# Optimization experiments

Measured on AMD Instinct MI355X. Metric: run time of the kernel, lower is better.

Reference implementation:

```python
import jax, jax.numpy as jnp
import numpy as np

B, T, NS, NC, M = 256, 128, 12, 4, 6
MU = 0.1                 # barrier parameter alg.mu
REG_BASE = 1.6           # fp.reg_exp_base
REG = 2.0                # bp.reg
REG_FAC = REG_BASE ** REG - 1.0


def _mt(a):
    return jnp.swapaxes(a, -1, -2)


def setup_inputs():
    key = jax.random.key(0)
    k = jax.random.split(key, 18)
    rn = lambda i, shape: jax.random.normal(k[i], shape, dtype=jnp.float32)
    eye_s = jnp.eye(NS, dtype=jnp.float32)
    eye_c = jnp.eye(NC, dtype=jnp.float32)
    fx = 0.9 * eye_s + 0.02 * rn(0, (B, T, NS, NS))
    fu = 0.1 * rn(1, (B, T, NS, NC))
    fxx = 0.01 * rn(2, (B, T, NS, NS, NS))
    fxu = 0.01 * rn(3, (B, T, NS, NS, NC))
    fuu = 0.01 * rn(4, (B, T, NS, NC, NC))
    qx = 0.1 * rn(5, (B, T, NS))
    qu = 0.1 * rn(6, (B, T, NC))
    Ax = 0.1 * rn(7, (B, T, NS, NS))
    qxx = eye_s + Ax @ _mt(Ax)            # PSD stage cost Hessian
    Au = 0.1 * rn(8, (B, T, NC, NC))
    quu = eye_c + Au @ _mt(Au)            # PD control Hessian
    qxu = 0.05 * rn(9, (B, T, NS, NC))
    cx = 0.1 * rn(10, (B, T, M, NS))
    cu = 0.1 * rn(11, (B, T, M, NC))
    # feasible iterate: c < 0 strictly, dual s > 0
    c = -(jax.random.uniform(k[12], (B, T, M), dtype=jnp.float32) + 0.1)
    s = 0.05 + 0.1 * jax.random.uniform(k[13], (B, T, M), dtype=jnp.float32)
    px = 0.1 * rn(14, (B, NS))
    P = 0.1 * rn(15, (B, NS, NS))
    pxx = eye_s + P @ _mt(P)              # PSD terminal Hessian
    return {"qx": qx, "qu": qu, "qxx": qxx, "qxu": qxu, "quu": quu,
            "fx": fx, "fu": fu, "fxx": fxx, "fxu": fxu, "fuu": fuu,
            "cx": cx, "cu": cu, "c": c, "s": s, "px": px, "pxx": pxx}


def _backward_pass(qx, qu, qxx, qxu, quu, fx, fu, fxx, fxu, fuu, cx, cu, c, s, px, pxx):
    """Feasible-branch ipddp Riccati backward recursion over T steps, batched over B."""
    Bsz = qx.shape[0]

    def step(carry, inp):
        Vx, Vxx, dV0, dV1, qu_err, mu_err = carry
        (qx_t, qu_t, qxx_t, qxu_t, quu_t, fx_t, fu_t,
         fxx_t, fxu_t, fuu_t, cx_t, cu_t, c_t, s_t) = inp
        s_col = s_t[..., None]                      # (B,M,1)
        c_col = c_t[..., None]                      # (B,M,1)
        # Q-function expansions
        Qx = qx_t[..., None] + _mt(cx_t) @ s_col + _mt(fx_t) @ Vx       # (B,NS,1)
        Qu = qu_t[..., None] + _mt(cu_t) @ s_col + _mt(fu_t) @ Vx       # (B,NC,1)
        fxV = _mt(fx_t) @ Vxx
        v = Vx[..., 0]                              # (B,NS)
        Qxx = qxx_t + fxV @ fx_t + jnp.einsum('bs,bsij->bij', v, fxx_t)
        Qxu = qxu_t + fxV @ fu_t + jnp.einsum('bs,bsij->bij', v, fxu_t)
        Quu = quu_t + _mt(fu_t) @ Vxx @ fu_t + jnp.einsum('bs,bsij->bij', v, fuu_t)
        Quu = 0.5 * (Quu + _mt(Quu))
        Quu_reg = Quu + quu_t * REG_FAC
        # interior-point (feasible) modifications
        r = s_col * c_col + MU                      # (B,M,1)
        cinv = 1.0 / c_col
        sc = (s_t / c_t)[..., None]                 # diag(SCinv) entries
        SCcu = sc * cu_t                            # SCinv @ cu
        SCcx = sc * cx_t                            # SCinv @ cx
        cuSCcu = _mt(cu_t) @ SCcu
        Qu = Qu - _mt(cu_t) @ (cinv * r)
        tempQux = _mt(Qxu) - _mt(cu_t) @ SCcx       # (B,NC,NS)
        rhs = jnp.concatenate([Qu, tempQux], axis=-1)   # (B,NC,1+NS)
        kK = -jnp.linalg.solve(Quu_reg - cuSCcu, rhs)
        ku = kK[..., :1]                            # (B,NC,1)
        Ku = kK[..., 1:]                            # (B,NC,NS)
        cuku = cu_t @ ku                            # (B,M,1)
        ks = (-cinv * (r + s_col * cuku))[..., 0]   # (B,M)
        Ks = -(sc * (cx_t + cu_t @ Ku))             # (B,M,NS)
        Quu2 = Quu - cuSCcu
        Qxu2 = _mt(tempQux)
        Qxx2 = Qxx - _mt(cx_t) @ SCcx
        Qx2 = Qx - _mt(cx_t) @ (cinv * r)
        dV0 = dV0 + (_mt(ku) @ Qu)[..., 0, 0]
        dV1 = dV1 + 0.5 * (_mt(ku) @ Quu2 @ ku)[..., 0, 0]
        QxuKu = Qxu2 @ Ku
        KtQ = _mt(Ku) @ Quu2
        Vx_new = Qx2 + _mt(Ku) @ Qu + KtQ @ ku + Qxu2 @ ku
        Vxx_new = Qxx2 + _mt(QxuKu) + QxuKu + KtQ @ Ku
        Vxx_new = 0.5 * (Vxx_new + _mt(Vxx_new))
        qu_err = jnp.maximum(qu_err, jnp.max(jnp.abs(Qu)))
        mu_err = jnp.maximum(mu_err, jnp.max(jnp.abs(r)))
        return (Vx_new, Vxx_new, dV0, dV1, qu_err, mu_err), (ku[..., 0], Ku, ks, Ks)

    xs = tuple(jnp.moveaxis(a, 1, 0) for a in
               (qx, qu, qxx, qxu, quu, fx, fu, fxx, fxu, fuu, cx, cu, c, s))
    zero = jnp.zeros((), jnp.float32)
    init = (px[..., None], pxx, jnp.zeros((Bsz,), jnp.float32),
            jnp.zeros((Bsz,), jnp.float32), zero, zero)
    carry, outs = jax.lax.scan(step, init, xs, reverse=True)
    Vx, Vxx, dV0, dV1, qu_err, mu_err = carry
    ku, Ku, ks, Ks = (jnp.moveaxis(o, 0, 1) for o in outs)
    dV = jnp.stack([dV0, dV1], axis=-1)             # (B,2)
    opterr = jnp.maximum(qu_err, mu_err)            # c_err == 0 in feasible branch
    return ku, Ku, ks, Ks, dV, opterr, Vx[..., 0], Vxx


def reference(qx, qu, qxx, qxu, quu, fx, fu, fxx, fxu, fuu, cx, cu, c, s, px, pxx):
    return _backward_pass(qx, qu, qxx, qxu, quu, fx, fu, fxx, fxu, fuu,
                          cx, cu, c, s, px, pxx)
```

## Files before the change

### kernel.cpp

```cpp
#include <hip/hip_runtime.h>
#include <cstdint>
#include <cstddef>

#define B_  256
#define T_  128
#define NS_ 12
#define NC_ 4
#define M_  6

constexpr float MU_F      = 0.1f;
constexpr float REG_FAC_F = (float)(1.6 * 1.6 - 1.0);

#define OF_FX   0
#define OF_FU   144
#define OF_FXX  192
#define OF_FXU  1920
#define OF_FUU  2496
#define OF_QXX  2688
#define OF_QXU  2832
#define OF_QUU  2880
#define OF_QX   2896
#define OF_QU   2908
#define OF_CX   2912
#define OF_CU   2984
#define OF_C    3008
#define OF_S    3014
#define STG_N   3020

#define O_KU    0
#define O_KUBIG 131072
#define O_KS    1703936
#define O_KSBIG 1900544
#define O_DV    4259840
#define O_OPT   4260352
#define O_VX    4260353
#define O_VXX   4263425

__device__ __forceinline__ void wsync_lds() {
    asm volatile("s_waitcnt lgkmcnt(0)" ::: "memory");
}
__device__ __forceinline__ void wsync_all() {
    asm volatile("s_waitcnt vmcnt(0) lgkmcnt(0)" ::: "memory");
}

__device__ __forceinline__ void gl_lds16(const float* g, float* l) {
    __builtin_amdgcn_global_load_lds((const __attribute__((address_space(1))) void*)g,
                                     (__attribute__((address_space(3))) void*)l, 16, 0, 0);
}
__device__ __forceinline__ void gl_lds4(const float* g, float* l) {
    __builtin_amdgcn_global_load_lds((const __attribute__((address_space(1))) void*)g,
                                     (__attribute__((address_space(3))) void*)l, 4, 0, 0);
}
__device__ __forceinline__ float4 ld4(const float* p)  { return *reinterpret_cast<const float4*>(p); }
__device__ __forceinline__ void   st4(float* p, float4 v) { *reinterpret_cast<float4*>(p) = v; }

__global__ __launch_bounds__(64) void ddp_backward(
    const float* __restrict__ qx,  const float* __restrict__ qu,
    const float* __restrict__ qxx, const float* __restrict__ qxu,
    const float* __restrict__ quu, const float* __restrict__ fx,
    const float* __restrict__ fu,  const float* __restrict__ fxx,
    const float* __restrict__ fxu, const float* __restrict__ fuu,
    const float* __restrict__ cx,  const float* __restrict__ cu,
    const float* __restrict__ c_,  const float* __restrict__ s_,
    const float* __restrict__ px,  const float* __restrict__ pxx,
    float* __restrict__ out, float* __restrict__ ws)
{
    const int l = threadIdx.x;
    const int b = blockIdx.x;

    __shared__ alignas(16) float stg[2][STG_N];
    __shared__ alignas(16) float sVxe[192];
    __shared__ alignas(16) float sG[192];
    __shared__ alignas(16) float sOUT[192];
    __shared__ alignas(16) float sQuuR[16], sQuu2[16], sM4[16];
    __shared__ alignas(16) float sQP[16];
    __shared__ alignas(16) float sKu[48];
    __shared__ alignas(16) float sku[4];
    __shared__ alignas(16) float sR[8], sCINV[8], sSC[8];
    __shared__ float sAcc[4];

    const float* srcs[14] = {qx, qu, qxx, qxu, quu, fx, fu, fxx, fxu, fuu, cx, cu, c_, s_};

    const int p   = l & 15, cq = l >> 4;
    const bool cq3 = (cq == 3);
    const int u1_x  = (p < 12) ? (OF_FX + p) : (OF_FU + p - 12);
    const int u1_xs = (p < 12) ? 12 : 4;
    const int u1_q0 = (p < 12) ? (OF_QX + p) : (OF_QU + p - 12);
    const int u1_w  = (p < 12) ? (OF_CX + p) : (OF_CU + p - 12);
    const int u1_ws = (p < 12) ? 12 : 4;
    const int pr = l >> 2, q4 = l & 3;
    const bool q43 = (q4 == 3);
    const int u2_q0 = (pr < 12) ? (q43 ? (OF_QXU + pr * 4) : (OF_QXX + pr * 12 + q4 * 4))
                                : (OF_QUU + (pr - 12) * 4);
    const int u2_x  = q43 ? OF_FU : (OF_FX + q4 * 4);
    const int u2_xs = q43 ? 4 : 12;
    const int u2_t  = (pr < 12) ? (q43 ? (OF_FXU + pr * 4) : (OF_FXX + pr * 12 + q4 * 4))
                                : (OF_FUU + (pr - 12) * 4);
    const int u2_ts = (pr < 12) ? (q43 ? 48 : 144) : 16;
    const int u2_w  = q43 ? OF_CU : (OF_CX + q4 * 4);
    const int u2_ws = q43 ? 4 : 12;
    const int i5 = l / 3, jq5 = l % 3;

    auto prefetch = [&](float* dst, int tt) {
        const uint32_t bt2 = (uint32_t)b * T_ + (uint32_t)tt;
        constexpr int ch_arr[22]  = {5,6,7,7,7,7,7,7,7,8,8,8,9,2,3,4,0,1,10,11,12,13};
        constexpr int ch_goff[22] = {0,0,0,256,512,768,1024,1280,1536,0,256,512,0,0,0,0,0,0,0,0,0,0};
        constexpr int ch_loff[22] = {OF_FX, OF_FU,
                                     OF_FXX, OF_FXX+256, OF_FXX+512, OF_FXX+768,
                                     OF_FXX+1024, OF_FXX+1280, OF_FXX+1536,
                                     OF_FXU, OF_FXU+256, OF_FXU+512,
                                     OF_FUU, OF_QXX, OF_QXU, OF_QUU, OF_QX, OF_QU,
                                     OF_CX, OF_CU, OF_C, OF_S};
        constexpr int ch_nb[22]   = {576,192,1024,1024,1024,1024,1024,1024,768,
                                     1024,1024,256,768,576,192,64,48,16,288,96,24,24};
        constexpr int sl[14]      = {12,4,144,48,16,144,48,1728,576,192,72,24,6,6};
        #pragma unroll
        for (int ci = 0; ci < 22; ++ci) {
            const uint32_t off = bt2 * (uint32_t)sl[ch_arr[ci]] + (uint32_t)ch_goff[ci];
            const float* g = srcs[ch_arr[ci]] + (size_t)off;
            float* dl = dst + ch_loff[ci];
            if ((ch_nb[ci] & 15) == 0) {
                if (l * 16 < ch_nb[ci]) gl_lds16(g + l * 4, dl);
            } else {
                if (l * 4  < ch_nb[ci]) gl_lds4 (g + l,     dl);
            }
        }
    };

    #pragma unroll
    for (int idx = l; idx < 192; idx += 64) {
        const int r = idx >> 4, ci = idx & 15;
        float v = 0.f;
        if (ci < 12)       v = pxx[(size_t)b * 144 + r * 12 + ci];
        else if (ci == 12) v = px[(size_t)b * 12 + r];
        sVxe[idx] = v;
    }
    prefetch(stg[0], T_ - 1);
    wsync_all();

    float dv0 = 0.f, dv1 = 0.f, qerr = 0.f, merr = 0.f;
    int cur = 0;
    for (int t = T_ - 1; t >= 0; --t) {
        const float* S = stg[cur];
        const uint32_t bt = (uint32_t)b * T_ + (uint32_t)t;

        float fcol[12];
        float4 vrow[12];
        #pragma unroll
        for (int m = 0; m < 12; ++m) fcol[m] = S[u1_x + m * u1_xs];
        #pragma unroll
        for (int m = 0; m < 12; ++m) vrow[m] = ld4(sVxe + m * 16 + cq * 4);
        const float4 csq0 = ld4(S + OF_C);
        const float4 csq1 = ld4(S + OF_C + 4);
        const float4 csq2 = ld4(S + OF_C + 8);
        float4 u2f[12];
        #pragma unroll
        for (int k = 0; k < 12; ++k) u2f[k] = ld4(S + u2_x + k * u2_xs);
        const float4 u2q0 = ld4(S + u2_q0);
        float4 u2tv[12];
        #pragma unroll
        for (int s2 = 0; s2 < 12; ++s2) u2tv[s2] = ld4(S + u2_t + s2 * u2_ts);

        if (t > 0) prefetch(stg[cur ^ 1], t - 1);

        {
            if (cq3 && p < 6) {
                const float cc = S[OF_C + p], sv = S[OF_S + p];
                sR[p]    = sv * cc + MU_F;
                sCINV[p] = 1.0f / cc;
                sSC[p]   = sv / cc;
            }
            float accx = 0.f, accy = 0.f, accz = 0.f, accw = 0.f;
            if (cq3) {
                float a0 = S[u1_q0];
                #pragma unroll
                for (int k = 0; k < 6; ++k) a0 += S[u1_w + k * u1_ws] * S[OF_S + k];
                accx = a0;
            }
            #pragma unroll
            for (int m = 0; m < 12; ++m) {
                const float f = fcol[m];
                accx += f * vrow[m].x; accy += f * vrow[m].y;
                accz += f * vrow[m].z; accw += f * vrow[m].w;
            }
            if (!cq3) {
                st4(sG + p * 12 + cq * 4, make_float4(accx, accy, accz, accw));
            } else {
                const float cv[6] = {csq0.x, csq0.y, csq0.z, csq0.w, csq1.x, csq1.y};
                const float sv[6] = {csq1.z, csq1.w, csq2.x, csq2.y, csq2.z, csq2.w};
                float rck[6], rrk[6];
                #pragma unroll
                for (int k = 0; k < 6; ++k) { rck[k] = 1.0f / cv[k]; rrk[k] = sv[k] * cv[k] + MU_F; }
                #pragma unroll
                for (int k = 0; k < 6; ++k) accx -= S[u1_w + k * u1_ws] * rck[k] * rrk[k];
                sQP[p] = accx;
            }
        }
        wsync_lds();

        {
            float vx[12];
            #pragma unroll
            for (int m = 0; m < 12; ++m) vx[m] = sVxe[m * 16 + 12];
            float rsc[6];
            #pragma unroll
            for (int k = 0; k < 6; ++k) rsc[k] = sSC[k];

            const float4 g0 = ld4(sG + pr * 12);
            const float4 g1 = ld4(sG + pr * 12 + 4);
            const float4 g2 = ld4(sG + pr * 12 + 8);
            const float gk[12] = {g0.x,g0.y,g0.z,g0.w, g1.x,g1.y,g1.z,g1.w, g2.x,g2.y,g2.z,g2.w};

            float4 acc = u2q0;
            #pragma unroll
            for (int k = 0; k < 12; ++k) {
                const float4 f = u2f[k];
                acc.x += gk[k]*f.x; acc.y += gk[k]*f.y; acc.z += gk[k]*f.z; acc.w += gk[k]*f.w;
            }
            #pragma unroll
            for (int s2 = 0; s2 < 12; ++s2) {
                const float4 tv = u2tv[s2];
                acc.x += vx[s2]*tv.x; acc.y += vx[s2]*tv.y; acc.z += vx[s2]*tv.z; acc.w += vx[s2]*tv.w;
            }
            if (pr < 12) {
                #pragma unroll
                for (int k = 0; k < 6; ++k) {
                    const float t2 = rsc[k] * S[OF_CX + k * 12 + pr];
                    const float4 cv = ld4(S + u2_w + k * u2_ws);
                    acc.x -= t2*cv.x; acc.y -= t2*cv.y; acc.z -= t2*cv.z; acc.w -= t2*cv.w;
                }
                st4(sOUT + pr * 16 + q4 * 4, acc);
            } else if (q43) {
                st4(sQuuR + (pr - 12) * 4, acc);
            }
            wsync_lds();
            if (pr >= 12 && q43) {
                const int a = pr - 12;
                const float accq[4] = {acc.x, acc.y, acc.z, acc.w};
                float q2v[4];
                #pragma unroll
                for (int bb = 0; bb < 4; ++bb) {
                    const float q = 0.5f * (accq[bb] + sQuuR[bb * 4 + a]);
                    float cs2 = 0.f;
                    #pragma unroll
                    for (int k = 0; k < 6; ++k)
                        cs2 += rsc[k] * S[OF_CU + k*4 + a] * S[OF_CU + k*4 + bb];
                    q2v[bb] = q - cs2;
                }
                const float4 quuq = ld4(S + OF_QUU + a * 4);
                st4(sQuu2 + a * 4, make_float4(q2v[0], q2v[1], q2v[2], q2v[3]));
                st4(sM4   + a * 4, make_float4(q2v[0] + quuq.x * REG_FAC_F,
                                               q2v[1] + quuq.y * REG_FAC_F,
                                               q2v[2] + quuq.z * REG_FAC_F,
                                               q2v[3] + quuq.w * REG_FAC_F));
            }
        }
        wsync_lds();

        if (l < 13) {
            float a00=sM4[0],  a01=sM4[1],  a02=sM4[2],  a03=sM4[3];
            float a10=sM4[4],  a11=sM4[5],  a12=sM4[6],  a13=sM4[7];
            float a20=sM4[8],  a21=sM4[9],  a22=sM4[10], a23=sM4[11];
            float a30=sM4[12], a31=sM4[13], a32=sM4[14], a33=sM4[15];
            const float i0 = 1.0f / a00;
            const float l10 = a10*i0, l20 = a20*i0, l30 = a30*i0;
            a11 -= l10*a01; a12 -= l10*a02; a13 -= l10*a03;
            a21 -= l20*a01; a22 -= l20*a02; a23 -= l20*a03;
            a31 -= l30*a01; a32 -= l30*a02; a33 -= l30*a03;
            const float i1 = 1.0f / a11;
            const float l21 = a21*i1, l31 = a31*i1;
            a22 -= l21*a12; a23 -= l21*a13;
            a32 -= l31*a12; a33 -= l31*a13;
            const float i2 = 1.0f / a22;
            const float l32 = a32*i2;
            a33 -= l32*a23;

            float r0, r1, r2, r3;
            if (l == 0) { const float4 q = ld4(sQP + 12);             r0=q.x; r1=q.y; r2=q.z; r3=q.w; }
            else        { const float4 q = ld4(sOUT + (l-1)*16 + 12); r0=q.x; r1=q.y; r2=q.z; r3=q.w; }

            const float y0 = r0;
            const float y1 = r1 - l10*y0;
            const float y2 = r2 - l20*y0 - l21*y1;
            const float y3 = r3 - l30*y0 - l31*y1 - l32*y2;
            float x3 = y3 / a33;
            float x2 = (y2 - a23*x3) * i2;
            float x1 = (y1 - a12*x2 - a13*x3) * i1;
            float x0 = (y0 - a01*x1 - a02*x2 - a03*x3) * i0;
            x0 = -x0; x1 = -x1; x2 = -x2; x3 = -x3;

            if (l == 0) {
                sku[0]=x0; sku[1]=x1; sku[2]=x2; sku[3]=x3;
                st4(out + O_KU + (size_t)bt * 4, make_float4(x0, x1, x2, x3));
                const float kux[4] = {x0, x1, x2, x3};
                float d0 = 0.f;
                #pragma unroll
                for (int a = 0; a < 4; ++a) d0 += kux[a] * sQP[12 + a];
                dv0 += d0;
                float d1 = 0.f;
                #pragma unroll
                for (int a = 0; a < 4; ++a)
                    #pragma unroll
                    for (int b2 = 0; b2 < 4; ++b2) d1 += kux[a] * sQuu2[a*4 + b2] * kux[b2];
                dv1 += 0.5f * d1;
            } else {
                const int i = l - 1;
                sKu[i]=x0; sKu[12+i]=x1; sKu[24+i]=x2; sKu[36+i]=x3;
                float* Kg = out + O_KUBIG + (size_t)bt * 48;
                Kg[i]=x0; Kg[12+i]=x1; Kg[24+i]=x2; Kg[36+i]=x3;
            }
        } else if (l == 20) {
            float m = 0.f;
            #pragma unroll
            for (int a = 0; a < 4; ++a) m = fmaxf(m, fabsf(sQP[12 + a]));
            qerr = fmaxf(qerr, m);
        } else if (l == 21) {
            float m = 0.f;
            #pragma unroll
            for (int k = 0; k < 6; ++k) m = fmaxf(m, fabsf(sR[k]));
            merr = fmaxf(merr, m);
        }
        wsync_lds();

        if (l < 18) {
            const int k = i5, iq = jq5;
            const float4 cxv = ld4(S + OF_CX + k*12 + iq*4);
            float a0 = cxv.x, a1 = cxv.y, a2 = cxv.z, a3v = cxv.w;
            #pragma unroll
            for (int a = 0; a < 4; ++a) {
                const float  cua = S[OF_CU + k*4 + a];
                const float4 kv  = ld4(sKu + a*12 + iq*4);
                a0 += cua*kv.x; a1 += cua*kv.y; a2 += cua*kv.z; a3v += cua*kv.w;
            }
            const float ns = -sSC[k];
            st4(out + O_KSBIG + (size_t)bt * 72 + k*12 + iq*4,
                make_float4(ns*a0, ns*a1, ns*a2, ns*a3v));
            if (iq == 0) {
                float cuku = 0.f;
                #pragma unroll
                for (int a = 0; a < 4; ++a) cuku += S[OF_CU + k*4 + a] * sku[a];
                out[O_KS + (size_t)bt * 6 + k] = -sCINV[k] * (sR[k] + S[OF_S + k] * cuku);
            }
        }
        if (l < 36) {
            const int i = i5, jq = jq5;
            const float4 v14  = ld4(sOUT + i*16 + jq*4);
            const float4 tqi4 = ld4(sOUT + i*16 + 12);
            const float tqi[4] = {tqi4.x, tqi4.y, tqi4.z, tqi4.w};
            float kuj[4][4], kui[4];
            #pragma unroll
            for (int a = 0; a < 4; ++a) {
                const float4 kv = ld4(sKu + a*12 + jq*4);
                kuj[a][0]=kv.x; kuj[a][1]=kv.y; kuj[a][2]=kv.z; kuj[a][3]=kv.w;
                kui[a] = sKu[a*12 + i];
            }
            float4 q2r[4];
            #pragma unroll
            for (int bb = 0; bb < 4; ++bb) q2r[bb] = ld4(sQuu2 + bb*4);
            float kqi[4] = {0.f, 0.f, 0.f, 0.f};
            #pragma unroll
            for (int bb = 0; bb < 4; ++bb) {
                kqi[0] += kui[bb]*q2r[bb].x; kqi[1] += kui[bb]*q2r[bb].y;
                kqi[2] += kui[bb]*q2r[bb].z; kqi[3] += kui[bb]*q2r[bb].w;
            }
            float kqj[4][4];
            #pragma unroll
            for (int r = 0; r < 4; ++r) { kqj[r][0]=0.f; kqj[r][1]=0.f; kqj[r][2]=0.f; kqj[r][3]=0.f; }
            #pragma unroll
            for (int bb = 0; bb < 4; ++bb) {
                #pragma unroll
                for (int r = 0; r < 4; ++r) {
                    kqj[r][0] += kuj[bb][r]*q2r[bb].x; kqj[r][1] += kuj[bb][r]*q2r[bb].y;
                    kqj[r][2] += kuj[bb][r]*q2r[bb].z; kqj[r][3] += kuj[bb][r]*q2r[bb].w;
                }
            }
            const float v1a[4] = {v14.x, v14.y, v14.z, v14.w};
            float v2[4], tqj[4][4];
            #pragma unroll
            for (int r = 0; r < 4; ++r) {
                const int j = jq*4 + r;
                v2[r] = sOUT[j*16 + i];
                const float4 tq = ld4(sOUT + j*16 + 12);
                tqj[r][0]=tq.x; tqj[r][1]=tq.y; tqj[r][2]=tq.z; tqj[r][3]=tq.w;
            }
            float res[4];
            #pragma unroll
            for (int r = 0; r < 4; ++r) {
                float qk = 0.f, kk1 = 0.f, kk2 = 0.f;
                #pragma unroll
                for (int a = 0; a < 4; ++a) {
                    qk  += tqi[a]*kuj[a][r] + tqj[r][a]*kui[a];
                    kk1 += kqi[a]*kuj[a][r];
                    kk2 += kqj[r][a]*kui[a];
                }
                res[r] = 0.5f*(v1a[r] + v2[r]) + qk + 0.5f*(kk1 + kk2);
            }
            st4(sVxe + i*16 + jq*4, make_float4(res[0], res[1], res[2], res[3]));
        } else if (l < 48) {
            const int i = l - 36;
            float kub[4];
            #pragma unroll
            for (int bb = 0; bb < 4; ++bb) kub[bb] = sKu[bb*12 + i];
            float4 q2r[4];
            #pragma unroll
            for (int bb = 0; bb < 4; ++bb) q2r[bb] = ld4(sQuu2 + bb*4);
            float ktq[4] = {0.f, 0.f, 0.f, 0.f};
            #pragma unroll
            for (int bb = 0; bb < 4; ++bb) {
                ktq[0] += kub[bb]*q2r[bb].x; ktq[1] += kub[bb]*q2r[bb].y;
                ktq[2] += kub[bb]*q2r[bb].z; ktq[3] += kub[bb]*q2r[bb].w;
            }
            float acc = sQP[i];
            #pragma unroll
            for (int a = 0; a < 4; ++a)
                acc += kub[a]*sQP[12+a] + ktq[a]*sku[a] + sOUT[i*16+12+a]*sku[a];
            st4(sVxe + i*16 + 12, make_float4(acc, 0.f, 0.f, 0.f));
        }
        wsync_all();
        cur ^= 1;
    }

    if (l == 20) sAcc[2] = qerr;
    if (l == 21) sAcc[3] = merr;
    wsync_lds();
    if (l == 0) {
        out[O_DV + b*2 + 0] = dv0;
        out[O_DV + b*2 + 1] = dv1;
        ws[b] = fmaxf(sAcc[2], sAcc[3]);
    }
    if (l < 12) out[O_VX + b*12 + l] = sVxe[l*16 + 12];
    #pragma unroll
    for (int idx = l; idx < 144; idx += 64)
        out[O_VXX + (size_t)b*144 + idx] = sVxe[(idx/12)*16 + (idx%12)];
}

__global__ __launch_bounds__(256) void opt_reduce(const float* __restrict__ ws,
                                                  float* __restrict__ out)
{
    float v = ws[threadIdx.x];
    #pragma unroll
    for (int o = 32; o > 0; o >>= 1) v = fmaxf(v, __shfl_down(v, o, 64));
    __shared__ float m[4];
    if ((threadIdx.x & 63) == 0) m[threadIdx.x >> 6] = v;
    __syncthreads();
    if (threadIdx.x == 0) out[O_OPT] = fmaxf(fmaxf(m[0], m[1]), fmaxf(m[2], m[3]));
}

extern "C" void kernel_launch(void* const* d_in, const int* in_sizes, int n_in,
                              void* d_out, int out_size, void* d_ws, size_t ws_size,
                              hipStream_t stream) {
    const float* qx  = (const float*)d_in[0];
    const float* qu  = (const float*)d_in[1];
    const float* qxx = (const float*)d_in[2];
    const float* qxu = (const float*)d_in[3];
    const float* quu = (const float*)d_in[4];
    const float* fx  = (const float*)d_in[5];
    const float* fu  = (const float*)d_in[6];
    const float* fxx = (const float*)d_in[7];
    const float* fxu = (const float*)d_in[8];
    const float* fuu = (const float*)d_in[9];
    const float* cx  = (const float*)d_in[10];
    const float* cu  = (const float*)d_in[11];
    const float* c_  = (const float*)d_in[12];
    const float* s_  = (const float*)d_in[13];
    const float* px  = (const float*)d_in[14];
    const float* pxx = (const float*)d_in[15];
    float* out = (float*)d_out;
    float* ws  = (float*)d_ws;

    hipLaunchKernelGGL(ddp_backward, dim3(B_), dim3(64), 0, stream,
                       qx, qu, qxx, qxu, quu, fx, fu, fxx, fxu, fuu,
                       cx, cu, c_, s_, px, pxx, out, ws);
    hipLaunchKernelGGL(opt_reduce, dim3(1), dim3(256), 0, stream, ws, out);
}
```

Before: 729.7 us.

## Split backward step into compute wave and prefetch/output wave per block

Launches two wavefronts per block. Wave 0 runs the serial Riccati critical path (Q expansion, 4x4 LU solve, Vxx update), while wave 1 issues the next timestep's global-to-LDS prefetch and writes the ks/Ks outputs, dV and error terms. Work is handed between waves with s_barrier. The aim is to take global memory issue and output stores off the latency-bound critical wave, at the cost of two block barriers per step and extra threads.

Result: faster. 691.2 us (-5.3%).

```diff
diff --git a/kernel.cpp b/kernel.cpp
--- a/kernel.cpp
+++ b/kernel.cpp
@@ -54,7 +54,7 @@
 __device__ __forceinline__ float4 ld4(const float* p)  { return *reinterpret_cast<const float4*>(p); }
 __device__ __forceinline__ void   st4(float* p, float4 v) { *reinterpret_cast<float4*>(p) = v; }
 
-__global__ __launch_bounds__(64) void ddp_backward(
+__global__ __launch_bounds__(128) void ddp_backward(
     const float* __restrict__ qx,  const float* __restrict__ qu,
     const float* __restrict__ qxx, const float* __restrict__ qxu,
     const float* __restrict__ quu, const float* __restrict__ fx,
@@ -65,14 +65,16 @@
     const float* __restrict__ px,  const float* __restrict__ pxx,
     float* __restrict__ out, float* __restrict__ ws)
 {
-    const int l = threadIdx.x;
-    const int b = blockIdx.x;
+    const int tid = threadIdx.x;
+    const int l   = tid & 63;
+    const int wv  = tid >> 6;
+    const int b   = blockIdx.x;
 
     __shared__ alignas(16) float stg[2][STG_N];
     __shared__ alignas(16) float sVxe[192];
     __shared__ alignas(16) float sG[192];
     __shared__ alignas(16) float sOUT[192];
-    __shared__ alignas(16) float sQuuR[16], sQuu2[16], sM4[16];
+    __shared__ alignas(16) float sQuu2[16], sM4[16];
     __shared__ alignas(16) float sQP[16];
     __shared__ alignas(16) float sKu[48];
     __shared__ alignas(16) float sku[4];
@@ -127,16 +129,21 @@
         }
     };
 
-    #pragma unroll
-    for (int idx = l; idx < 192; idx += 64) {
-        const int r = idx >> 4, ci = idx & 15;
-        float v = 0.f;
-        if (ci < 12)       v = pxx[(size_t)b * 144 + r * 12 + ci];
-        else if (ci == 12) v = px[(size_t)b * 12 + r];
-        sVxe[idx] = v;
+    if (wv == 0) {
+        #pragma unroll
+        for (int idx = l; idx < 192; idx += 64) {
+            const int r = idx >> 4, ci = idx & 15;
+            float v = 0.f;
+            if (ci < 12)       v = pxx[(size_t)b * 144 + r * 12 + ci];
+            else if (ci == 12) v = px[(size_t)b * 12 + r];
+            sVxe[idx] = v;
+        }
+        wsync_lds();
+    } else {
+        prefetch(stg[0], T_ - 1);
+        wsync_all();
     }
-    prefetch(stg[0], T_ - 1);
-    wsync_all();
+    __builtin_amdgcn_s_barrier();
 
     float dv0 = 0.f, dv1 = 0.f, qerr = 0.f, merr = 0.f;
     int cur = 0;
@@ -144,294 +151,314 @@
         const float* S = stg[cur];
         const uint32_t bt = (uint32_t)b * T_ + (uint32_t)t;
 
-        float fcol[12];
-        float4 vrow[12];
-        #pragma unroll
-        for (int m = 0; m < 12; ++m) fcol[m] = S[u1_x + m * u1_xs];
-        #pragma unroll
-        for (int m = 0; m < 12; ++m) vrow[m] = ld4(sVxe + m * 16 + cq * 4);
-        const float4 csq0 = ld4(S + OF_C);
-        const float4 csq1 = ld4(S + OF_C + 4);
-        const float4 csq2 = ld4(S + OF_C + 8);
-        float4 u2f[12];
-        #pragma unroll
-        for (int k = 0; k < 12; ++k) u2f[k] = ld4(S + u2_x + k * u2_xs);
-        const float4 u2q0 = ld4(S + u2_q0);
-        float4 u2tv[12];
-        #pragma unroll
-        for (int s2 = 0; s2 < 12; ++s2) u2tv[s2] = ld4(S + u2_t + s2 * u2_ts);
-
-        if (t > 0) prefetch(stg[cur ^ 1], t - 1);
-
-        {
-            if (cq3 && p < 6) {
-                const float cc = S[OF_C + p], sv = S[OF_S + p];
-                sR[p]    = sv * cc + MU_F;
-                sCINV[p] = 1.0f / cc;
-                sSC[p]   = sv / cc;
-            }
-            float accx = 0.f, accy = 0.f, accz = 0.f, accw = 0.f;
-            if (cq3) {
-                float a0 = S[u1_q0];
-                #pragma unroll
-                for (int k = 0; k < 6; ++k) a0 += S[u1_w + k * u1_ws] * S[OF_S + k];
-                accx = a0;
-            }
+        if (wv == 1) {
+            if (t > 0) prefetch(stg[cur ^ 1], t - 1);
+        } else {
+            float fcol[12];
+            float4 vrow[12];
             #pragma unroll
-            for (int m = 0; m < 12; ++m) {
-                const float f = fcol[m];
-                accx += f * vrow[m].x; accy += f * vrow[m].y;
-                accz += f * vrow[m].z; accw += f * vrow[m].w;
-            }
-            if (!cq3) {
-                st4(sG + p * 12 + cq * 4, make_float4(accx, accy, accz, accw));
-            } else {
-                const float cv[6] = {csq0.x, csq0.y, csq0.z, csq0.w, csq1.x, csq1.y};
-                const float sv[6] = {csq1.z, csq1.w, csq2.x, csq2.y, csq2.z, csq2.w};
-                float rck[6], rrk[6];
-                #pragma unroll
-                for (int k = 0; k < 6; ++k) { rck[k] = 1.0f / cv[k]; rrk[k] = sv[k] * cv[k] + MU_F; }
-                #pragma unroll
-                for (int k = 0; k < 6; ++k) accx -= S[u1_w + k * u1_ws] * rck[k] * rrk[k];
-                sQP[p] = accx;
-            }
+            for (int m = 0; m < 12; ++m) fcol[m] = S[u1_x + m * u1_xs];
+            #pragma unroll
+            for (int m = 0; m < 12; ++m) vrow[m] = ld4(sVxe + m * 16 + cq * 4);
+            const float4 csq0 = ld4(S + OF_C);
+            const float4 csq1 = ld4(S + OF_C + 4);
+            const float4 csq2 = ld4(S + OF_C + 8);
+            float4 u2f[12];
+            #pragma unroll
+            for (int k = 0; k < 12; ++k) u2f[k] = ld4(S + u2_x + k * u2_xs);
+            const float4 u2q0 = ld4(S + u2_q0);
+            float4 u2tv[12];
+            #pragma unroll
+            for (int s2 = 0; s2 < 12; ++s2) u2tv[s2] = ld4(S + u2_t + s2 * u2_ts);
+
+            {
+                if (cq3 && p < 6) {
+                    const float cc = S[OF_C + p], sv = S[OF_S + p];
+                    sR[p]    = sv * cc + MU_F;
+                    sCINV[p] = 1.0f / cc;
+                    sSC[p]   = sv / cc;
+                }
+                float accx = 0.f, accy = 0.f, accz = 0.f, accw = 0.f;
+                if (cq3) {
+                    float a0 = S[u1_q0];
+                    #pragma unroll
+                    for (int k = 0; k < 6; ++k) a0 += S[u1_w + k * u1_ws] * S[OF_S + k];
+                    accx = a0;
+                }
+                #pragma unroll
+                for (int m = 0; m < 12; ++m) {
+                    const float f = fcol[m];
+                    accx += f * vrow[m].x; accy += f * vrow[m].y;
+                    accz += f * vrow[m].z; accw += f * vrow[m].w;
+                }
+                if (!cq3) {
+                    st4(sG + p * 12 + cq * 4, make_float4(accx, accy, accz, accw));
+                } else {
+                    const float cv6[6] = {csq0.x, csq0.y, csq0.z, csq0.w, csq1.x, csq1.y};
+                    const float sv6[6] = {csq1.z, csq1.w, csq2.x, csq2.y, csq2.z, csq2.w};
+                    float rck[6], rrk[6];
+                    #pragma unroll
+                    for (int k = 0; k < 6; ++k) { rck[k] = 1.0f / cv6[k]; rrk[k] = sv6[k] * cv6[k] + MU_F; }
+                    #pragma unroll
+                    for (int k = 0; k < 6; ++k) accx -= S[u1_w + k * u1_ws] * rck[k] * rrk[k];
+                    sQP[p] = accx;
+                }
+            }
+            wsync_lds();
+
+            {
+                float vx[12];
+                #pragma unroll
+                for (int m = 0; m < 12; ++m) vx[m] = sVxe[m * 16 + 12];
+                float rsc[6];
+                #pragma unroll
+                for (int k = 0; k < 6; ++k) rsc[k] = sSC[k];
+
+                const float4 g0 = ld4(sG + pr * 12);
+                const float4 g1 = ld4(sG + pr * 12 + 4);
+                const float4 g2 = ld4(sG + pr * 12 + 8);
+                const float gk[12] = {g0.x,g0.y,g0.z,g0.w, g1.x,g1.y,g1.z,g1.w, g2.x,g2.y,g2.z,g2.w};
+
+                float4 acc = u2q0;
+                #pragma unroll
+                for (int k = 0; k < 12; ++k) {
+                    const float4 f = u2f[k];
+                    acc.x += gk[k]*f.x; acc.y += gk[k]*f.y; acc.z += gk[k]*f.z; acc.w += gk[k]*f.w;
+                }
+                #pragma unroll
+                for (int s2 = 0; s2 < 12; ++s2) {
+                    const float4 tv = u2tv[s2];
+                    acc.x += vx[s2]*tv.x; acc.y += vx[s2]*tv.y; acc.z += vx[s2]*tv.z; acc.w += vx[s2]*tv.w;
+                }
+                if (pr < 12) {
+                    #pragma unroll
+                    for (int k = 0; k < 6; ++k) {
+                        const float t2 = rsc[k] * S[OF_CX + k * 12 + pr];
+                        const float4 cv = ld4(S + u2_w + k * u2_ws);
+                        acc.x -= t2*cv.x; acc.y -= t2*cv.y; acc.z -= t2*cv.z; acc.w -= t2*cv.w;
+                    }
+                    st4(sOUT + pr * 16 + q4 * 4, acc);
+                } else if (q43) {
+                    const int a = pr - 12;
+                    const float accq[4] = {acc.x, acc.y, acc.z, acc.w};
+                    float q2v[4];
+                    #pragma unroll
+                    for (int bb = 0; bb < 4; ++bb) {
+                        float cacc = S[OF_QUU + bb*4 + a];
+                        #pragma unroll
+                        for (int k = 0; k < 12; ++k)
+                            cacc += sG[(12 + bb) * 12 + k] * S[OF_FU + k*4 + a];
+                        #pragma unroll
+                        for (int s2 = 0; s2 < 12; ++s2)
+                            cacc += vx[s2] * S[OF_FUU + s2*16 + bb*4 + a];
+                        const float q = 0.5f * (accq[bb] + cacc);
+                        float cs2 = 0.f;
+                        #pragma unroll
+                        for (int k = 0; k < 6; ++k)
+                            cs2 += rsc[k] * S[OF_CU + k*4 + a] * S[OF_CU + k*4 + bb];
+                        q2v[bb] = q - cs2;
+                    }
+                    const float4 quuq = ld4(S + OF_QUU + a * 4);
+                    st4(sQuu2 + a * 4, make_float4(q2v[0], q2v[1], q2v[2], q2v[3]));
+                    st4(sM4   + a * 4, make_float4(q2v[0] + quuq.x * REG_FAC_F,
+                                                   q2v[1] + quuq.y * REG_FAC_F,
+                                                   q2v[2] + quuq.z * REG_FAC_F,
+                                                   q2v[3] + quuq.w * REG_FAC_F));
+                }
+            }
+            wsync_lds();
+
+            if (l < 13) {
+                float a00=sM4[0],  a01=sM4[1],  a02=sM4[2],  a03=sM4[3];
+                float a10=sM4[4],  a11=sM4[5],  a12=sM4[6],  a13=sM4[7];
+                float a20=sM4[8],  a21=sM4[9],  a22=sM4[10], a23=sM4[11];
+                float a30=sM4[12], a31=sM4[13], a32=sM4[14], a33=sM4[15];
+                const float i0 = 1.0f / a00;
+                const float l10 = a10*i0, l20 = a20*i0, l30 = a30*i0;
+                a11 -= l10*a01; a12 -= l10*a02; a13 -= l10*a03;
+                a21 -= l20*a01; a22 -= l20*a02; a23 -= l20*a03;
+                a31 -= l30*a01; a32 -= l30*a02; a33 -= l30*a03;
+                const float i1 = 1.0f / a11;
+                const float l21 = a21*i1, l31 = a31*i1;
+                a22 -= l21*a12; a23 -= l21*a13;
+                a32 -= l31*a12; a33 -= l31*a13;
+                const float i2 = 1.0f / a22;
+                const float l32 = a32*i2;
+                a33 -= l32*a23;
+
+                float r0, r1, r2, r3;
+                if (l == 0) { const float4 q = ld4(sQP + 12);             r0=q.x; r1=q.y; r2=q.z; r3=q.w; }
+                else        { const float4 q = ld4(sOUT + (l-1)*16 + 12); r0=q.x; r1=q.y; r2=q.z; r3=q.w; }
+
+                const float y0 = r0;
+                const float y1 = r1 - l10*y0;
+                const float y2 = r2 - l20*y0 - l21*y1;
+                const float y3 = r3 - l30*y0 - l31*y1 - l32*y2;
+                float x3 = y3 / a33;
+                float x2 = (y2 - a23*x3) * i2;
+                float x1 = (y1 - a12*x2 - a13*x3) * i1;
+                float x0 = (y0 - a01*x1 - a02*x2 - a03*x3) * i0;
+                x0 = -x0; x1 = -x1; x2 = -x2; x3 = -x3;
+
+                if (l == 0) { sku[0]=x0; sku[1]=x1; sku[2]=x2; sku[3]=x3; }
+                else {
+                    const int i = l - 1;
+                    sKu[i]=x0; sKu[12+i]=x1; sKu[24+i]=x2; sKu[36+i]=x3;
+                }
+            }
+            wsync_lds();
         }
-        wsync_lds();
-
-        {
-            float vx[12];
-            #pragma unroll
-            for (int m = 0; m < 12; ++m) vx[m] = sVxe[m * 16 + 12];
-            float rsc[6];
-            #pragma unroll
-            for (int k = 0; k < 6; ++k) rsc[k] = sSC[k];
-
-            const float4 g0 = ld4(sG + pr * 12);
-            const float4 g1 = ld4(sG + pr * 12 + 4);
-            const float4 g2 = ld4(sG + pr * 12 + 8);
-            const float gk[12] = {g0.x,g0.y,g0.z,g0.w, g1.x,g1.y,g1.z,g1.w, g2.x,g2.y,g2.z,g2.w};
-
-            float4 acc = u2q0;
-            #pragma unroll
-            for (int k = 0; k < 12; ++k) {
-                const float4 f = u2f[k];
-                acc.x += gk[k]*f.x; acc.y += gk[k]*f.y; acc.z += gk[k]*f.z; acc.w += gk[k]*f.w;
-            }
-            #pragma unroll
-            for (int s2 = 0; s2 < 12; ++s2) {
-                const float4 tv = u2tv[s2];
-                acc.x += vx[s2]*tv.x; acc.y += vx[s2]*tv.y; acc.z += vx[s2]*tv.z; acc.w += vx[s2]*tv.w;
-            }
-            if (pr < 12) {
-                #pragma unroll
-                for (int k = 0; k < 6; ++k) {
-                    const float t2 = rsc[k] * S[OF_CX + k * 12 + pr];
-                    const float4 cv = ld4(S + u2_w + k * u2_ws);
-                    acc.x -= t2*cv.x; acc.y -= t2*cv.y; acc.z -= t2*cv.z; acc.w -= t2*cv.w;
-                }
-                st4(sOUT + pr * 16 + q4 * 4, acc);
-            } else if (q43) {
-                st4(sQuuR + (pr - 12) * 4, acc);
+        __builtin_amdgcn_s_barrier();
+
+        if (wv == 0) {
+            if (l < 36) {
+                const int i = i5, jq = jq5;
+                const float4 v14  = ld4(sOUT + i*16 + jq*4);
+                const float4 tqi4 = ld4(sOUT + i*16 + 12);
+                const float tqi[4] = {tqi4.x, tqi4.y, tqi4.z, tqi4.w};
+                float kuj[4][4], kui[4];
+                #pragma unroll
+                for (int a = 0; a < 4; ++a) {
+                    const float4 kv = ld4(sKu + a*12 + jq*4);
+                    kuj[a][0]=kv.x; kuj[a][1]=kv.y; kuj[a][2]=kv.z; kuj[a][3]=kv.w;
+                    kui[a] = sKu[a*12 + i];
+                }
+                float4 q2r[4];
+                #pragma unroll
+                for (int bb = 0; bb < 4; ++bb) q2r[bb] = ld4(sQuu2 + bb*4);
+                float kqi[4] = {0.f, 0.f, 0.f, 0.f};
+                #pragma unroll
+                for (int bb = 0; bb < 4; ++bb) {
+                    kqi[0] += kui[bb]*q2r[bb].x; kqi[1] += kui[bb]*q2r[bb].y;
+                    kqi[2] += kui[bb]*q2r[bb].z; kqi[3] += kui[bb]*q2r[bb].w;
+                }
+                float kqj[4][4];
+                #pragma unroll
+                for (int r = 0; r < 4; ++r) { kqj[r][0]=0.f; kqj[r][1]=0.f; kqj[r][2]=0.f; kqj[r][3]=0.f; }
+                #pragma unroll
+                for (int bb = 0; bb < 4; ++bb) {
+                    #pragma unroll
+                    for (int r = 0; r < 4; ++r) {
+                        kqj[r][0] += kuj[bb][r]*q2r[bb].x; kqj[r][1] += kuj[bb][r]*q2r[bb].y;
+                        kqj[r][2] += kuj[bb][r]*q2r[bb].z; kqj[r][3] += kuj[bb][r]*q2r[bb].w;
+                    }
+                }
+                const float v1a[4] = {v14.x, v14.y, v14.z, v14.w};
+                float v2[4], tqj[4][4];
+                #pragma unroll
+                for (int r = 0; r < 4; ++r) {
+                    const int j = jq*4 + r;
+                    v2[r] = sOUT[j*16 + i];
+                    const float4 tq = ld4(sOUT + j*16 + 12);
+                    tqj[r][0]=tq.x; tqj[r][1]=tq.y; tqj[r][2]=tq.z; tqj[r][3]=tq.w;
+                }
+                float res[4];
+                #pragma unroll
+                for (int r = 0; r < 4; ++r) {
+                    float qk = 0.f, kk1 = 0.f, kk2 = 0.f;
+                    #pragma unroll
+                    for (int a = 0; a < 4; ++a) {
+                        qk  += tqi[a]*kuj[a][r] + tqj[r][a]*kui[a];
+                        kk1 += kqi[a]*kuj[a][r];
+                        kk2 += kqj[r][a]*kui[a];
+                    }
+                    res[r] = 0.5f*(v1a[r] + v2[r]) + qk + 0.5f*(kk1 + kk2);
+                }
+                st4(sVxe + i*16 + jq*4, make_float4(res[0], res[1], res[2], res[3]));
+            } else if (l < 48) {
+                const int i = l - 36;
+                float kub[4];
+                #pragma unroll
+                for (int bb = 0; bb < 4; ++bb) kub[bb] = sKu[bb*12 + i];
+                float4 q2r[4];
+                #pragma unroll
+                for (int bb = 0; bb < 4; ++bb) q2r[bb] = ld4(sQuu2 + bb*4);
+                float ktq[4] = {0.f, 0.f, 0.f, 0.f};
+                #pragma unroll
+                for (int bb = 0; bb < 4; ++bb) {
+                    ktq[0] += kub[bb]*q2r[bb].x; ktq[1] += kub[bb]*q2r[bb].y;
+                    ktq[2] += kub[bb]*q2r[bb].z; ktq[3] += kub[bb]*q2r[bb].w;
+                }
+                float acc = sQP[i];
+                #pragma unroll
+                for (int a = 0; a < 4; ++a)
+                    acc += kub[a]*sQP[12+a] + ktq[a]*sku[a] + sOUT[i*16+12+a]*sku[a];
+                st4(sVxe + i*16 + 12, make_float4(acc, 0.f, 0.f, 0.f));
             }
             wsync_lds();
-            if (pr >= 12 && q43) {
-                const int a = pr - 12;
-                const float accq[4] = {acc.x, acc.y, acc.z, acc.w};
-                float q2v[4];
-                #pragma unroll
-                for (int bb = 0; bb < 4; ++bb) {
-                    const float q = 0.5f * (accq[bb] + sQuuR[bb * 4 + a]);
-                    float cs2 = 0.f;
-                    #pragma unroll
-                    for (int k = 0; k < 6; ++k)
-                        cs2 += rsc[k] * S[OF_CU + k*4 + a] * S[OF_CU + k*4 + bb];
-                    q2v[bb] = q - cs2;
-                }
-                const float4 quuq = ld4(S + OF_QUU + a * 4);
-                st4(sQuu2 + a * 4, make_float4(q2v[0], q2v[1], q2v[2], q2v[3]));
-                st4(sM4   + a * 4, make_float4(q2v[0] + quuq.x * REG_FAC_F,
-                                               q2v[1] + quuq.y * REG_FAC_F,
-                                               q2v[2] + quuq.z * REG_FAC_F,
-                                               q2v[3] + quuq.w * REG_FAC_F));
-            }
-        }
-        wsync_lds();
-
-        if (l < 13) {
-            float a00=sM4[0],  a01=sM4[1],  a02=sM4[2],  a03=sM4[3];
-            float a10=sM4[4],  a11=sM4[5],  a12=sM4[6],  a13=sM4[7];
-            float a20=sM4[8],  a21=sM4[9],  a22=sM4[10], a23=sM4[11];
-            float a30=sM4[12], a31=sM4[13], a32=sM4[14], a33=sM4[15];
-            const float i0 = 1.0f / a00;
-            const float l10 = a10*i0, l20 = a20*i0, l30 = a30*i0;
-            a11 -= l10*a01; a12 -= l10*a02; a13 -= l10*a03;
-            a21 -= l20*a01; a22 -= l20*a02; a23 -= l20*a03;
-            a31 -= l30*a01; a32 -= l30*a02; a33 -= l30*a03;
-            const float i1 = 1.0f / a11;
-            const float l21 = a21*i1, l31 = a31*i1;
-            a22 -= l21*a12; a23 -= l21*a13;
-            a32 -= l31*a12; a33 -= l31*a13;
-            const float i2 = 1.0f / a22;
-            const float l32 = a32*i2;
-            a33 -= l32*a23;
-
-            float r0, r1, r2, r3;
-            if (l == 0) { const float4 q = ld4(sQP + 12);             r0=q.x; r1=q.y; r2=q.z; r3=q.w; }
-            else        { const float4 q = ld4(sOUT + (l-1)*16 + 12); r0=q.x; r1=q.y; r2=q.z; r3=q.w; }
-
-            const float y0 = r0;
-            const float y1 = r1 - l10*y0;
-            const float y2 = r2 - l20*y0 - l21*y1;
-            const float y3 = r3 - l30*y0 - l31*y1 - l32*y2;
-            float x3 = y3 / a33;
-            float x2 = (y2 - a23*x3) * i2;
-            float x1 = (y1 - a12*x2 - a13*x3) * i1;
-            float x0 = (y0 - a01*x1 - a02*x2 - a03*x3) * i0;
-            x0 = -x0; x1 = -x1; x2 = -x2; x3 = -x3;
-
-            if (l == 0) {
-                sku[0]=x0; sku[1]=x1; sku[2]=x2; sku[3]=x3;
-                st4(out + O_KU + (size_t)bt * 4, make_float4(x0, x1, x2, x3));
-                const float kux[4] = {x0, x1, x2, x3};
+        } else {
+            if (l == 40) {
+                st4(out + O_KU + (size_t)bt * 4, ld4(sku));
+            } else if (l > 40 && l <= 52) {
+                const int i = l - 41;
+                float* Kg = out + O_KUBIG + (size_t)bt * 48;
+                Kg[i]    = sKu[i];
+                Kg[12+i] = sKu[12+i];
+                Kg[24+i] = sKu[24+i];
+                Kg[36+i] = sKu[36+i];
+            }
+            if (l < 18) {
+                const int k = i5, iq = jq5;
+                const float4 cxv = ld4(S + OF_CX + k*12 + iq*4);
+                float a0 = cxv.x, a1 = cxv.y, a2 = cxv.z, a3v = cxv.w;
+                #pragma unroll
+                for (int a = 0; a < 4; ++a) {
+                    const float  cua = S[OF_CU + k*4 + a];
+                    const float4 kv  = ld4(sKu + a*12 + iq*4);
+                    a0 += cua*kv.x; a1 += cua*kv.y; a2 += cua*kv.z; a3v += cua*kv.w;
+                }
+                const float ns = -sSC[k];
+                st4(out + O_KSBIG + (size_t)bt * 72 + k*12 + iq*4,
+                    make_float4(ns*a0, ns*a1, ns*a2, ns*a3v));
+                if (iq == 0) {
+                    float cuku = 0.f;
+                    #pragma unroll
+                    for (int a = 0; a < 4; ++a) cuku += S[OF_CU + k*4 + a] * sku[a];
+                    out[O_KS + (size_t)bt * 6 + k] = -sCINV[k] * (sR[k] + S[OF_S + k] * cuku);
+                }
+            } else if (l == 32) {
                 float d0 = 0.f;
                 #pragma unroll
-                for (int a = 0; a < 4; ++a) d0 += kux[a] * sQP[12 + a];
+                for (int a = 0; a < 4; ++a) d0 += sku[a] * sQP[12 + a];
                 dv0 += d0;
                 float d1 = 0.f;
                 #pragma unroll
                 for (int a = 0; a < 4; ++a)
                     #pragma unroll
-                    for (int b2 = 0; b2 < 4; ++b2) d1 += kux[a] * sQuu2[a*4 + b2] * kux[b2];
+                    for (int b2 = 0; b2 < 4; ++b2) d1 += sku[a] * sQuu2[a*4 + b2] * sku[b2];
                 dv1 += 0.5f * d1;
-            } else {
-                const int i = l - 1;
-                sKu[i]=x0; sKu[12+i]=x1; sKu[24+i]=x2; sKu[36+i]=x3;
-                float* Kg = out + O_KUBIG + (size_t)bt * 48;
-                Kg[i]=x0; Kg[12+i]=x1; Kg[24+i]=x2; Kg[36+i]=x3;
-            }
-        } else if (l == 20) {
-            float m = 0.f;
-            #pragma unroll
-            for (int a = 0; a < 4; ++a) m = fmaxf(m, fabsf(sQP[12 + a]));
-            qerr = fmaxf(qerr, m);
-        } else if (l == 21) {
-            float m = 0.f;
-            #pragma unroll
-            for (int k = 0; k < 6; ++k) m = fmaxf(m, fabsf(sR[k]));
-            merr = fmaxf(merr, m);
+            } else if (l == 33) {
+                float m = 0.f;
+                #pragma unroll
+                for (int a = 0; a < 4; ++a) m = fmaxf(m, fabsf(sQP[12 + a]));
+                qerr = fmaxf(qerr, m);
+            } else if (l == 34) {
+                float m = 0.f;
+                #pragma unroll
+                for (int k = 0; k < 6; ++k) m = fmaxf(m, fabsf(sR[k]));
+                merr = fmaxf(merr, m);
+            }
+            wsync_all();
         }
-        wsync_lds();
-
-        if (l < 18) {
-            const int k = i5, iq = jq5;
-            const float4 cxv = ld4(S + OF_CX + k*12 + iq*4);
-            float a0 = cxv.x, a1 = cxv.y, a2 = cxv.z, a3v = cxv.w;
-            #pragma unroll
-            for (int a = 0; a < 4; ++a) {
-                const float  cua = S[OF_CU + k*4 + a];
-                const float4 kv  = ld4(sKu + a*12 + iq*4);
-                a0 += cua*kv.x; a1 += cua*kv.y; a2 += cua*kv.z; a3v += cua*kv.w;
-            }
-            const float ns = -sSC[k];
-            st4(out + O_KSBIG + (size_t)bt * 72 + k*12 + iq*4,
-                make_float4(ns*a0, ns*a1, ns*a2, ns*a3v));
-            if (iq == 0) {
-                float cuku = 0.f;
-                #pragma unroll
-                for (int a = 0; a < 4; ++a) cuku += S[OF_CU + k*4 + a] * sku[a];
-                out[O_KS + (size_t)bt * 6 + k] = -sCINV[k] * (sR[k] + S[OF_S + k] * cuku);
-            }
-        }
-        if (l < 36) {
-            const int i = i5, jq = jq5;
-            const float4 v14  = ld4(sOUT + i*16 + jq*4);
-            const float4 tqi4 = ld4(sOUT + i*16 + 12);
-            const float tqi[4] = {tqi4.x, tqi4.y, tqi4.z, tqi4.w};
-            float kuj[4][4], kui[4];
-            #pragma unroll
-            for (int a = 0; a < 4; ++a) {
-                const float4 kv = ld4(sKu + a*12 + jq*4);
-                kuj[a][0]=kv.x; kuj[a][1]=kv.y; kuj[a][2]=kv.z; kuj[a][3]=kv.w;
-                kui[a] = sKu[a*12 + i];
-            }
-            float4 q2r[4];
-            #pragma unroll
-            for (int bb = 0; bb < 4; ++bb) q2r[bb] = ld4(sQuu2 + bb*4);
-            float kqi[4] = {0.f, 0.f, 0.f, 0.f};
-            #pragma unroll
-            for (int bb = 0; bb < 4; ++bb) {
-                kqi[0] += kui[bb]*q2r[bb].x; kqi[1] += kui[bb]*q2r[bb].y;
-                kqi[2] += kui[bb]*q2r[bb].z; kqi[3] += kui[bb]*q2r[bb].w;
-            }
-            float kqj[4][4];
-            #pragma unroll
-            for (int r = 0; r < 4; ++r) { kqj[r][0]=0.f; kqj[r][1]=0.f; kqj[r][2]=0.f; kqj[r][3]=0.f; }
-            #pragma unroll
-            for (int bb = 0; bb < 4; ++bb) {
-                #pragma unroll
-                for (int r = 0; r < 4; ++r) {
-                    kqj[r][0] += kuj[bb][r]*q2r[bb].x; kqj[r][1] += kuj[bb][r]*q2r[bb].y;
-                    kqj[r][2] += kuj[bb][r]*q2r[bb].z; kqj[r][3] += kuj[bb][r]*q2r[bb].w;
-                }
-            }
-            const float v1a[4] = {v14.x, v14.y, v14.z, v14.w};
-            float v2[4], tqj[4][4];
-            #pragma unroll
-            for (int r = 0; r < 4; ++r) {
-                const int j = jq*4 + r;
-                v2[r] = sOUT[j*16 + i];
-                const float4 tq = ld4(sOUT + j*16 + 12);
-                tqj[r][0]=tq.x; tqj[r][1]=tq.y; tqj[r][2]=tq.z; tqj[r][3]=tq.w;
-            }
-            float res[4];
-            #pragma unroll
-            for (int r = 0; r < 4; ++r) {
-                float qk = 0.f, kk1 = 0.f, kk2 = 0.f;
-                #pragma unroll
-                for (int a = 0; a < 4; ++a) {
-                    qk  += tqi[a]*kuj[a][r] + tqj[r][a]*kui[a];
-                    kk1 += kqi[a]*kuj[a][r];
-                    kk2 += kqj[r][a]*kui[a];
-                }
-                res[r] = 0.5f*(v1a[r] + v2[r]) + qk + 0.5f*(kk1 + kk2);
-            }
-            st4(sVxe + i*16 + jq*4, make_float4(res[0], res[1], res[2], res[3]));
-        } else if (l < 48) {
-            const int i = l - 36;
-            float kub[4];
-            #pragma unroll
-            for (int bb = 0; bb < 4; ++bb) kub[bb] = sKu[bb*12 + i];
-            float4 q2r[4];
-            #pragma unroll
-            for (int bb = 0; bb < 4; ++bb) q2r[bb] = ld4(sQuu2 + bb*4);
-            float ktq[4] = {0.f, 0.f, 0.f, 0.f};
-            #pragma unroll
-            for (int bb = 0; bb < 4; ++bb) {
-                ktq[0] += kub[bb]*q2r[bb].x; ktq[1] += kub[bb]*q2r[bb].y;
-                ktq[2] += kub[bb]*q2r[bb].z; ktq[3] += kub[bb]*q2r[bb].w;
-            }
-            float acc = sQP[i];
-            #pragma unroll
-            for (int a = 0; a < 4; ++a)
-                acc += kub[a]*sQP[12+a] + ktq[a]*sku[a] + sOUT[i*16+12+a]*sku[a];
-            st4(sVxe + i*16 + 12, make_float4(acc, 0.f, 0.f, 0.f));
-        }
-        wsync_all();
+        __builtin_amdgcn_s_barrier();
         cur ^= 1;
     }
 
-    if (l == 20) sAcc[2] = qerr;
-    if (l == 21) sAcc[3] = merr;
-    wsync_lds();
-    if (l == 0) {
-        out[O_DV + b*2 + 0] = dv0;
-        out[O_DV + b*2 + 1] = dv1;
-        ws[b] = fmaxf(sAcc[2], sAcc[3]);
+    if (wv == 0) {
+        if (l < 12) out[O_VX + b*12 + l] = sVxe[l*16 + 12];
+        #pragma unroll
+        for (int idx = l; idx < 144; idx += 64)
+            out[O_VXX + (size_t)b*144 + idx] = sVxe[(idx/12)*16 + (idx%12)];
+    } else {
+        if (l == 33) sAcc[2] = qerr;
+        if (l == 34) sAcc[3] = merr;
+        wsync_lds();
+        if (l == 32) {
+            out[O_DV + b*2 + 0] = dv0;
+            out[O_DV + b*2 + 1] = dv1;
+        }
+        if (l == 33) ws[b] = fmaxf(sAcc[2], sAcc[3]);
     }
-    if (l < 12) out[O_VX + b*12 + l] = sVxe[l*16 + 12];
-    #pragma unroll
-    for (int idx = l; idx < 144; idx += 64)
-        out[O_VXX + (size_t)b*144 + idx] = sVxe[(idx/12)*16 + (idx%12)];
 }
 
 __global__ __launch_bounds__(256) void opt_reduce(const float* __restrict__ ws,
@@ -468,7 +495,7 @@
     float* out = (float*)d_out;
     float* ws  = (float*)d_ws;
 
-    hipLaunchKernelGGL(ddp_backward, dim3(B_), dim3(64), 0, stream,
+    hipLaunchKernelGGL(ddp_backward, dim3(B_), dim3(128), 0, stream,
                        qx, qu, qxx, qxu, quu, fx, fu, fxx, fxu, fuu,
                        cx, cu, c_, s_, px, pxx, out, ws);
     hipLaunchKernelGGL(opt_reduce, dim3(1), dim3(256), 0, stream, ws, out);
```
